# Optimization experiments

Hardware: AMD Instinct MI355X
Metric: run time of the kernel (lower is better)

The kernel has to match this reference:

```python
import jax, jax.numpy as jnp
import numpy as np

VOXEL_SIZE = np.array([0.05, 0.05, 0.1], np.float32)
PC_RANGE = np.array([0.0, -40.0, -3.0, 70.4, 40.0, 1.0], np.float32)
GRID = np.round((PC_RANGE[3:] - PC_RANGE[:3]) / VOXEL_SIZE).astype(np.int64)  # (x,y,z) = (1408,1600,40)
MAX_POINTS = 35
MAX_VOXELS = 60000
N_POINTS = 2_000_000
NDIM = 4


def setup_inputs() -> dict:
    key = jax.random.key(0)
    k1, k2 = jax.random.split(key)
    span = jnp.asarray(PC_RANGE[3:] - PC_RANGE[:3])
    lo = jnp.asarray(PC_RANGE[:3])
    # uniform xyz inside the point-cloud range (slight overshoot ok; out-of-range points get dropped)
    xyz = jax.random.uniform(k1, (N_POINTS, 3), jnp.float32) * span * 1.02 + lo - 0.01 * span
    feat = jax.random.uniform(k2, (N_POINTS, NDIM - 3), jnp.float32)
    return {"points": jnp.concatenate([xyz, feat], axis=1)}


def hard_voxelize(points):
    """Faithful jit-able hard voxelization.

    Returns fixed-size (padded) outputs plus voxel_num, instead of the
    dynamically-sliced outputs of the CUDA kernel (data-dependent shapes are
    not jit-compatible). voxels[:voxel_num], coors[:voxel_num],
    num_points_per_voxel[:voxel_num] match the kernel semantics: voxels are
    numbered in order of first point appearance, points fill a voxel in
    arrival order, overflow points/voxels are dropped.
    """
    n = points.shape[0]
    gx, gy, gz = int(GRID[0]), int(GRID[1]), int(GRID[2])
    c = jnp.floor((points[:, :3] - jnp.asarray(PC_RANGE[:3])) / jnp.asarray(VOXEL_SIZE)).astype(jnp.int32)
    in_range = jnp.all((c >= 0) & (c < jnp.array([gx, gy, gz], jnp.int32)), axis=1)
    big = gx * gy * gz  # sentinel linear id for invalid points
    lin = jnp.where(in_range, (c[:, 2] * gy + c[:, 1]) * gx + c[:, 0], big)

    order = jnp.argsort(lin)  # stable: preserves arrival order within a voxel
    slin = lin[order]
    sc = c[order]
    spts = points[order]

    newg = jnp.concatenate([jnp.ones((1,), bool), slin[1:] != slin[:-1]])
    gid = jnp.cumsum(newg) - 1  # group id per sorted point (sorted-lin order)
    ar = jnp.arange(n, dtype=jnp.int32)

    grp_start = jnp.full((n,), n, jnp.int32).at[gid].min(ar)                      # sorted pos of first pt in group
    first_orig = jnp.full((n,), n, jnp.int32).at[gid].min(order.astype(jnp.int32))  # first-appearance index
    grp_valid = (jnp.zeros((n,), jnp.int32).at[gid].max((slin != big).astype(jnp.int32))) > 0

    # voxel ids assigned in order of first appearance (invalid groups pushed last)
    first_key = jnp.where(grp_valid, first_orig, n)
    perm = jnp.argsort(first_key)
    vid_of_group = jnp.zeros((n,), jnp.int32).at[perm].set(ar)

    pos = ar - grp_start[gid]          # arrival rank of point within its voxel
    vid_pt = vid_of_group[gid]
    keep = (slin != big) & (vid_pt < MAX_VOXELS) & (pos < MAX_POINTS)
    vi = jnp.where(keep, vid_pt, MAX_VOXELS)  # out-of-range -> dropped by scatter
    pi = jnp.where(keep, pos, 0)
    voxels = jnp.zeros((MAX_VOXELS, MAX_POINTS, points.shape[1]), points.dtype).at[vi, pi].set(spts, mode='drop')

    counts = jnp.zeros((n,), jnp.int32).at[gid].add((slin != big).astype(jnp.int32))
    g_ok = grp_valid & (vid_of_group < MAX_VOXELS)
    gv = jnp.where(g_ok, vid_of_group, MAX_VOXELS)
    numpv = jnp.zeros((MAX_VOXELS,), jnp.int32).at[gv].set(jnp.minimum(counts, MAX_POINTS), mode='drop')

    coors_g = sc[jnp.minimum(grp_start, n - 1)][:, ::-1]  # stored as (z, y, x) like the kernel
    coors = jnp.zeros((MAX_VOXELS, 3), jnp.int32).at[gv].set(coors_g, mode='drop')

    voxel_num = jnp.minimum(jnp.sum(grp_valid.astype(jnp.int32)), MAX_VOXELS)
    return voxels, coors, numpv, voxel_num


def reference(points):
    return hard_voxelize(points)
```

## Files before the change

### kernel.cpp

```cpp
#include <hip/hip_runtime.h>

constexpr int GX = 1408, GY = 1600, GZ = 40;
constexpr float LOX = 0.0f, LOY = -40.0f, LOZ = -3.0f;
constexpr float VSX = 0.05f, VSY = 0.05f, VSZ = 0.1f;
constexpr int MAXV = 60000, MAXP = 35;
constexpr int LINBITS = 27;
constexpr unsigned LINMASK = (1u << LINBITS) - 1;
constexpr unsigned EMPTYK = 0xFFFFFFFFu;
constexpr unsigned VINIT  = 0x7FFFFFFFu;

constexpr int NBIN   = 2048;
constexpr int LSLOT  = 2048;
constexpr int BINCAP = 1536;
constexpr int BPT    = 1024;
constexpr int PPB    = 8192;
constexpr int RND    = PPB / BPT;
constexpr int HPT    = BINCAP / 256;

constexpr int NCAND = 131072;
constexpr int NCB   = NCAND / 16384;

constexpr size_t CO_OFF = (size_t)MAXV * MAXP * 4;
constexpr size_t NP_OFF = CO_OFF + (size_t)MAXV * 3;
constexpr size_t VN_OFF = NP_OFF + (size_t)MAXV;

__device__ __forceinline__ unsigned hash22(unsigned lin) {
    return (lin * 2654435761u) >> 10;
}

__global__ __launch_bounds__(1024) void k_bin(const float4* __restrict__ pts, int n,
                                              unsigned long long* __restrict__ binbuf,
                                              int* __restrict__ bincnt) {
    __shared__ int cnt[NBIN], gbase[NBIN];
    int t = threadIdx.x;
    for (int b = t; b < NBIN; b += BPT) cnt[b] = 0;
    __syncthreads();

    unsigned lin[RND];
    unsigned rb[RND];
    int base = blockIdx.x * PPB;
    #pragma unroll
    for (int k = 0; k < RND; ++k) {
        int i = base + k * BPT + t;
        rb[k] = 0xFFFFFFFFu;
        if (i < n) {
            float4 p = pts[i];
            float fx = floorf((p.x - LOX) / VSX);
            float fy = floorf((p.y - LOY) / VSY);
            float fz = floorf((p.z - LOZ) / VSZ);
            if (fx >= 0.f && fy >= 0.f && fz >= 0.f &&
                fx < (float)GX && fy < (float)GY && fz < (float)GZ) {
                unsigned lv = ((unsigned)(int)fz * GY + (unsigned)(int)fy) * GX
                            + (unsigned)(int)fx;
                unsigned b = hash22(lv) >> 11;
                unsigned r = (unsigned)atomicAdd(&cnt[b], 1);
                rb[k] = (b << 16) | r;
                lin[k] = lv;
            }
        }
    }
    __syncthreads();
    for (int b = t; b < NBIN; b += BPT)
        if (cnt[b] > 0) gbase[b] = atomicAdd(&bincnt[b], cnt[b]);
    __syncthreads();
    #pragma unroll
    for (int k = 0; k < RND; ++k) {
        if (rb[k] != 0xFFFFFFFFu) {
            unsigned b = rb[k] >> 16;
            int d = gbase[b] + (int)(rb[k] & 0xFFFFu);
            unsigned i = (unsigned)(base + k * BPT + t);
            if (d < BINCAP)
                binbuf[(size_t)b * BINCAP + d] =
                    ((unsigned long long)i << LINBITS) | lin[k];
        }
    }
}

__device__ __forceinline__ unsigned lds_insert32(unsigned* kt, unsigned* vt,
                                                 unsigned lin, unsigned idx) {
    unsigned h = hash22(lin) & (LSLOT - 1);
    while (true) {
        unsigned k = kt[h];
        if (k == EMPTYK) {
            unsigned old = atomicCAS(&kt[h], EMPTYK, lin);
            if (old == EMPTYK || old == lin) { atomicMin(&vt[h], idx); return h; }
            k = old;
        }
        if (k == lin) { atomicMin(&vt[h], idx); return h; }
        h = (h + 1) & (LSLOT - 1);
    }
}

__global__ __launch_bounds__(256) void k_flags2(const unsigned long long* __restrict__ binbuf,
                                                const int* __restrict__ bincnt,
                                                unsigned char* __restrict__ flagbyte,
                                                int* __restrict__ dcount) {
    __shared__ unsigned kt[LSLOT], vt[LSLOT];
    int t = threadIdx.x, bin = blockIdx.x;
    for (int s = t; s < LSLOT; s += 256) { kt[s] = EMPTYK; vt[s] = VINIT; }
    __syncthreads();
    int cnt = min(bincnt[bin], BINCAP);
    const unsigned long long* buf = binbuf + (size_t)bin * BINCAP;
    for (int j = t; j < cnt; j += 256) {
        unsigned long long e = buf[j];
        lds_insert32(kt, vt, (unsigned)(e & LINMASK), (unsigned)(e >> LINBITS));
    }
    __syncthreads();
    int occ = 0;
    for (int s = t; s < LSLOT; s += 256) {
        if (kt[s] != EMPTYK) {
            ++occ;
            unsigned fi = vt[s];
            if (fi < (unsigned)NCAND) flagbyte[fi] = 1;
        }
    }
    for (int o = 1; o < 64; o <<= 1) occ += __shfl_xor(occ, o);
    __shared__ int ws[4];
    int lane = t & 63, wid = t >> 6;
    if (lane == 0) ws[wid] = occ;
    __syncthreads();
    if (t == 0) atomicAdd(dcount, ws[0] + ws[1] + ws[2] + ws[3]);
}

__device__ __forceinline__ unsigned nib(unsigned v) {
    return (v & 1u) | ((v >> 7) & 2u) | ((v >> 14) & 4u) | ((v >> 21) & 8u);
}

__global__ __launch_bounds__(256) void k_pack(const uint4* __restrict__ fb4,
                                              unsigned* __restrict__ flagw,
                                              int* __restrict__ wsums) {
    int gt = blockIdx.x * 256 + threadIdx.x;
    uint4 q0 = fb4[gt * 4 + 0], q1 = fb4[gt * 4 + 1];
    uint4 q2 = fb4[gt * 4 + 2], q3 = fb4[gt * 4 + 3];
    unsigned w0 = nib(q0.x) | (nib(q0.y) << 4) | (nib(q0.z) << 8)  | (nib(q0.w) << 12)
                | (nib(q1.x) << 16) | (nib(q1.y) << 20) | (nib(q1.z) << 24) | (nib(q1.w) << 28);
    unsigned w1 = nib(q2.x) | (nib(q2.y) << 4) | (nib(q2.z) << 8)  | (nib(q2.w) << 12)
                | (nib(q3.x) << 16) | (nib(q3.y) << 20) | (nib(q3.z) << 24) | (nib(q3.w) << 28);
    flagw[gt * 2]     = w0;
    flagw[gt * 2 + 1] = w1;
    int pc = __popc(w0) + __popc(w1);
    for (int o = 1; o < 64; o <<= 1) pc += __shfl_xor(pc, o);
    __shared__ int ws[4];
    int lane = threadIdx.x & 63, wid = threadIdx.x >> 6;
    if (lane == 0) ws[wid] = pc;
    __syncthreads();
    if (threadIdx.x == 0) wsums[blockIdx.x] = ws[0] + ws[1] + ws[2] + ws[3];
}

__global__ __launch_bounds__(256) void k_wbase(const unsigned* __restrict__ flagw,
                                               const int* __restrict__ wsums,
                                               int* __restrict__ wordbase,
                                               int nb3, const int* __restrict__ dcount,
                                               float* __restrict__ vn_out) {
    __shared__ int sh[256];
    int t = threadIdx.x;
    int v = (t < nb3) ? wsums[t] : 0;
    sh[t] = v;
    __syncthreads();
    for (int o = 1; o < 256; o <<= 1) {
        int u = (t >= o) ? sh[t - o] : 0;
        __syncthreads();
        sh[t] += u;
        __syncthreads();
    }
    int blkbase = (blockIdx.x == 0) ? 0 : sh[blockIdx.x - 1];
    if (blockIdx.x == 0 && t == 0)
        vn_out[0] = (float)min(dcount[0], MAXV);
    __syncthreads();
    int gt = blockIdx.x * 256 + t;
    unsigned w0 = flagw[gt * 2], w1 = flagw[gt * 2 + 1];
    int p0 = __popc(w0);
    int mysum = p0 + __popc(w1);
    sh[t] = mysum;
    __syncthreads();
    for (int o = 1; o < 256; o <<= 1) {
        int u = (t >= o) ? sh[t - o] : 0;
        __syncthreads();
        sh[t] += u;
        __syncthreads();
    }
    int excl = sh[t] - mysum + blkbase;
    wordbase[gt * 2]     = excl;
    wordbase[gt * 2 + 1] = excl + p0;
}

__global__ __launch_bounds__(256) void k_fill2(const unsigned long long* __restrict__ binbuf,
                                               const int* __restrict__ bincnt,
                                               const unsigned* __restrict__ flagw,
                                               const int* __restrict__ wordbase,
                                               int* __restrict__ cursor,
                                               int* __restrict__ lists,
                                               float* __restrict__ coors_out) {
    __shared__ unsigned kt[LSLOT], vt[LSLOT];
    int t = threadIdx.x, bin = blockIdx.x;
    for (int s = t; s < LSLOT; s += 256) { kt[s] = EMPTYK; vt[s] = VINIT; }
    __syncthreads();
    int cnt = min(bincnt[bin], BINCAP);
    const unsigned long long* buf = binbuf + (size_t)bin * BINCAP;
    unsigned hmem[HPT];
    #pragma unroll
    for (int q = 0; q < HPT; ++q) {
        int j = t + q * 256;
        hmem[q] = 0;
        if (j < cnt) {
            unsigned long long e = buf[j];
            hmem[q] = lds_insert32(kt, vt, (unsigned)(e & LINMASK),
                                   (unsigned)(e >> LINBITS));
        }
    }
    __syncthreads();
    for (int s = t; s < LSLOT; s += 256) {
        unsigned k = kt[s];
        if (k == EMPTYK) continue;
        unsigned fi = vt[s];
        unsigned vid = (unsigned)MAXV;
        if (fi < (unsigned)NCAND) {
            unsigned w = flagw[fi >> 5];
            vid = (unsigned)wordbase[fi >> 5]
                + (unsigned)__popc(w & ((1u << (fi & 31)) - 1u));
        }
        vt[s] = vid;
        if (vid < (unsigned)MAXV) {
            int x = (int)(k % (unsigned)GX);
            unsigned tq = k / (unsigned)GX;
            coors_out[(size_t)vid * 3 + 0] = (float)(tq / (unsigned)GY);
            coors_out[(size_t)vid * 3 + 1] = (float)(tq % (unsigned)GY);
            coors_out[(size_t)vid * 3 + 2] = (float)x;
        }
    }
    __syncthreads();
    #pragma unroll
    for (int q = 0; q < HPT; ++q) {
        int j = t + q * 256;
        if (j < cnt) {
            unsigned vid = vt[hmem[q]];
            if (vid < (unsigned)MAXV) {
                unsigned i = (unsigned)(buf[j] >> LINBITS);
                int pos = atomicAdd(&cursor[vid], 1);
                if (pos < MAXP) lists[vid * MAXP + pos] = (int)i;
            }
        }
    }
}

constexpr int VPB = 7;
__global__ __launch_bounds__(256) void k_write(const int* __restrict__ cursor,
                                               const int* __restrict__ lists,
                                               const float4* __restrict__ pts,
                                               float* __restrict__ vox_out,
                                               float* __restrict__ np_out) {
    __shared__ int sidx[VPB * MAXP];
    __shared__ int scnt[VPB];
    int t = threadIdx.x;
    int lv = t / MAXP;
    int r  = t - lv * MAXP;
    int v  = blockIdx.x * VPB + lv;
    bool act = (t < VPB * MAXP) && (v < MAXV);
    if (act && r == 0) scnt[lv] = min(cursor[v], MAXP);
    __syncthreads();
    int k = 0, myidx = 0x7fffffff;
    if (act) {
        k = scnt[lv];
        if (r < k) myidx = lists[v * MAXP + r];
        sidx[lv * MAXP + r] = myidx;
    }
    __syncthreads();
    if (!act) return;
    float4 val = make_float4(0.f, 0.f, 0.f, 0.f);
    int rank = r;
    if (r < k) {
        rank = 0;
        for (int j = 0; j < k; ++j) rank += (sidx[lv * MAXP + j] < myidx);
        val = pts[myidx];
    }
    ((float4*)vox_out)[(size_t)v * MAXP + rank] = val;
    if (r == 0) np_out[v] = (float)k;
}

extern "C" void kernel_launch(void* const* d_in, const int* in_sizes, int n_in,
                              void* d_out, int out_size, void* d_ws, size_t ws_size,
                              hipStream_t stream) {
    const float4* pts = (const float4*)d_in[0];
    int n = in_sizes[0] / 4;
    float* out = (float*)d_out;
    char* ws = (char*)d_ws;
    int nbin_blk = (n + PPB - 1) / PPB;

    size_t off = 0;
    unsigned char* flagbyte = (unsigned char*)(ws + off);
    off += (size_t)NCAND;
    int* cursor = (int*)(ws + off);
    off += (size_t)MAXV * 4;
    int* bincnt = (int*)(ws + off);
    off += (size_t)NBIN * 4;
    int* dcount = (int*)(ws + off);
    off += 256;
    size_t zero_bytes = off;
    off = (off + 255) & ~(size_t)255;
    unsigned long long* binbuf = (unsigned long long*)(ws + off);
    off += (size_t)NBIN * BINCAP * 8;
    unsigned* flagw = (unsigned*)(ws + off);
    off += (size_t)NCB * 512 * 4;
    int* wordbase = (int*)(ws + off);
    off += (size_t)NCB * 512 * 4;
    int* wsums = (int*)(ws + off);
    off += 1024;
    int* lists = (int*)(ws + off);

    hipMemsetAsync(flagbyte, 0, zero_bytes, stream);
    hipMemsetAsync(out + CO_OFF, 0, (size_t)(out_size - (int)CO_OFF) * 4, stream);

    k_bin   <<<nbin_blk, BPT, 0, stream>>>(pts, n, binbuf, bincnt);
    k_flags2<<<NBIN, 256, 0, stream>>>(binbuf, bincnt, flagbyte, dcount);
    k_pack  <<<NCB, 256, 0, stream>>>((const uint4*)flagbyte, flagw, wsums);
    k_wbase <<<NCB, 256, 0, stream>>>(flagw, wsums, wordbase, NCB, dcount, out + VN_OFF);
    k_fill2 <<<NBIN, 256, 0, stream>>>(binbuf, bincnt, flagw, wordbase,
                                       cursor, lists, out + CO_OFF);
    k_write <<<(MAXV + VPB - 1) / VPB, 256, 0, stream>>>(cursor, lists, pts,
                                                         out, out + NP_OFF);
}
```

Before: 176.6 us.

## Persist per-point first-index from hash pass and merge flag pack/scan into one kernel

The first hash-table pass now writes each point's voxel first-appearance index to a global per-bin array, so the fill kernel no longer rebuilds the LDS hash table and just looks up the voxel id per point. The flag packing and the two-level prefix scan are merged into a single one-block kernel, which cuts one launch. In exchange it adds an extra 4-byte global write and read per binned point, and the scan now runs on a single workgroup.

New measurement: 165.4 us. -6.3%, faster.

```diff
diff --git a/kernel.cpp b/kernel.cpp
--- a/kernel.cpp
+++ b/kernel.cpp
@@ -18,7 +18,6 @@
 constexpr int HPT    = BINCAP / 256;
 
 constexpr int NCAND = 131072;
-constexpr int NCB   = NCAND / 16384;
 
 constexpr size_t CO_OFF = (size_t)MAXV * MAXP * 4;
 constexpr size_t NP_OFF = CO_OFF + (size_t)MAXV * 3;
@@ -91,19 +90,29 @@
     }
 }
 
-__global__ __launch_bounds__(256) void k_flags2(const unsigned long long* __restrict__ binbuf,
-                                                const int* __restrict__ bincnt,
-                                                unsigned char* __restrict__ flagbyte,
-                                                int* __restrict__ dcount) {
+__global__ __launch_bounds__(256) void k_tab(const unsigned long long* __restrict__ binbuf,
+                                             const int* __restrict__ bincnt,
+                                             unsigned char* __restrict__ flagbyte,
+                                             unsigned* __restrict__ pfirst,
+                                             int* __restrict__ dcount) {
     __shared__ unsigned kt[LSLOT], vt[LSLOT];
+    __shared__ int ws4[4];
     int t = threadIdx.x, bin = blockIdx.x;
+    int lane = t & 63, wid = t >> 6;
     for (int s = t; s < LSLOT; s += 256) { kt[s] = EMPTYK; vt[s] = VINIT; }
     __syncthreads();
     int cnt = min(bincnt[bin], BINCAP);
     const unsigned long long* buf = binbuf + (size_t)bin * BINCAP;
-    for (int j = t; j < cnt; j += 256) {
-        unsigned long long e = buf[j];
-        lds_insert32(kt, vt, (unsigned)(e & LINMASK), (unsigned)(e >> LINBITS));
+    unsigned mem[HPT];
+    #pragma unroll
+    for (int q = 0; q < HPT; ++q) {
+        int j = t + q * 256;
+        mem[q] = 0;
+        if (j < cnt) {
+            unsigned long long e = buf[j];
+            mem[q] = lds_insert32(kt, vt, (unsigned)(e & LINMASK),
+                                  (unsigned)(e >> LINBITS));
+        }
     }
     __syncthreads();
     int occ = 0;
@@ -115,47 +124,40 @@
         }
     }
     for (int o = 1; o < 64; o <<= 1) occ += __shfl_xor(occ, o);
-    __shared__ int ws[4];
-    int lane = t & 63, wid = t >> 6;
-    if (lane == 0) ws[wid] = occ;
-    __syncthreads();
-    if (t == 0) atomicAdd(dcount, ws[0] + ws[1] + ws[2] + ws[3]);
+    if (lane == 0) ws4[wid] = occ;
+    unsigned* pf = pfirst + (size_t)bin * BINCAP;
+    #pragma unroll
+    for (int q = 0; q < HPT; ++q) {
+        int j = t + q * 256;
+        if (j < cnt) pf[j] = vt[mem[q]];
+    }
+    __syncthreads();
+    if (t == 0) atomicAdd(dcount, ws4[0] + ws4[1] + ws4[2] + ws4[3]);
 }
 
 __device__ __forceinline__ unsigned nib(unsigned v) {
     return (v & 1u) | ((v >> 7) & 2u) | ((v >> 14) & 4u) | ((v >> 21) & 8u);
 }
 
-__global__ __launch_bounds__(256) void k_pack(const uint4* __restrict__ fb4,
-                                              unsigned* __restrict__ flagw,
-                                              int* __restrict__ wsums) {
-    int gt = blockIdx.x * 256 + threadIdx.x;
-    uint4 q0 = fb4[gt * 4 + 0], q1 = fb4[gt * 4 + 1];
-    uint4 q2 = fb4[gt * 4 + 2], q3 = fb4[gt * 4 + 3];
-    unsigned w0 = nib(q0.x) | (nib(q0.y) << 4) | (nib(q0.z) << 8)  | (nib(q0.w) << 12)
-                | (nib(q1.x) << 16) | (nib(q1.y) << 20) | (nib(q1.z) << 24) | (nib(q1.w) << 28);
-    unsigned w1 = nib(q2.x) | (nib(q2.y) << 4) | (nib(q2.z) << 8)  | (nib(q2.w) << 12)
-                | (nib(q3.x) << 16) | (nib(q3.y) << 20) | (nib(q3.z) << 24) | (nib(q3.w) << 28);
-    flagw[gt * 2]     = w0;
-    flagw[gt * 2 + 1] = w1;
-    int pc = __popc(w0) + __popc(w1);
-    for (int o = 1; o < 64; o <<= 1) pc += __shfl_xor(pc, o);
-    __shared__ int ws[4];
-    int lane = threadIdx.x & 63, wid = threadIdx.x >> 6;
-    if (lane == 0) ws[wid] = pc;
-    __syncthreads();
-    if (threadIdx.x == 0) wsums[blockIdx.x] = ws[0] + ws[1] + ws[2] + ws[3];
-}
-
-__global__ __launch_bounds__(256) void k_wbase(const unsigned* __restrict__ flagw,
-                                               const int* __restrict__ wsums,
+__global__ __launch_bounds__(256) void k_scan1(const uint4* __restrict__ fb4,
+                                               unsigned* __restrict__ flagw,
                                                int* __restrict__ wordbase,
-                                               int nb3, const int* __restrict__ dcount,
+                                               const int* __restrict__ dcount,
                                                float* __restrict__ vn_out) {
     __shared__ int sh[256];
     int t = threadIdx.x;
-    int v = (t < nb3) ? wsums[t] : 0;
-    sh[t] = v;
+    unsigned w[16];
+    int mysum = 0;
+    int b4 = t * 32;
+    #pragma unroll
+    for (int k = 0; k < 16; ++k) {
+        uint4 a = fb4[b4 + 2 * k], b = fb4[b4 + 2 * k + 1];
+        unsigned wk = nib(a.x) | (nib(a.y) << 4) | (nib(a.z) << 8)  | (nib(a.w) << 12)
+                    | (nib(b.x) << 16) | (nib(b.y) << 20) | (nib(b.z) << 24) | (nib(b.w) << 28);
+        w[k] = wk;
+        mysum += __popc(wk);
+    }
+    sh[t] = mysum;
     __syncthreads();
     for (int o = 1; o < 256; o <<= 1) {
         int u = (t >= o) ? sh[t - o] : 0;
@@ -163,83 +165,47 @@
         sh[t] += u;
         __syncthreads();
     }
-    int blkbase = (blockIdx.x == 0) ? 0 : sh[blockIdx.x - 1];
-    if (blockIdx.x == 0 && t == 0)
-        vn_out[0] = (float)min(dcount[0], MAXV);
-    __syncthreads();
-    int gt = blockIdx.x * 256 + t;
-    unsigned w0 = flagw[gt * 2], w1 = flagw[gt * 2 + 1];
-    int p0 = __popc(w0);
-    int mysum = p0 + __popc(w1);
-    sh[t] = mysum;
-    __syncthreads();
-    for (int o = 1; o < 256; o <<= 1) {
-        int u = (t >= o) ? sh[t - o] : 0;
-        __syncthreads();
-        sh[t] += u;
-        __syncthreads();
-    }
-    int excl = sh[t] - mysum + blkbase;
-    wordbase[gt * 2]     = excl;
-    wordbase[gt * 2 + 1] = excl + p0;
-}
-
-__global__ __launch_bounds__(256) void k_fill2(const unsigned long long* __restrict__ binbuf,
+    int run = sh[t] - mysum;
+    if (t == 0) vn_out[0] = (float)min(dcount[0], MAXV);
+    #pragma unroll
+    for (int k = 0; k < 16; ++k) {
+        flagw[t * 16 + k] = w[k];
+        wordbase[t * 16 + k] = run;
+        run += __popc(w[k]);
+    }
+}
+
+__global__ __launch_bounds__(256) void k_fill3(const unsigned long long* __restrict__ binbuf,
                                                const int* __restrict__ bincnt,
+                                               const unsigned* __restrict__ pfirst,
                                                const unsigned* __restrict__ flagw,
                                                const int* __restrict__ wordbase,
                                                int* __restrict__ cursor,
                                                int* __restrict__ lists,
                                                float* __restrict__ coors_out) {
-    __shared__ unsigned kt[LSLOT], vt[LSLOT];
     int t = threadIdx.x, bin = blockIdx.x;
-    for (int s = t; s < LSLOT; s += 256) { kt[s] = EMPTYK; vt[s] = VINIT; }
-    __syncthreads();
     int cnt = min(bincnt[bin], BINCAP);
     const unsigned long long* buf = binbuf + (size_t)bin * BINCAP;
-    unsigned hmem[HPT];
-    #pragma unroll
-    for (int q = 0; q < HPT; ++q) {
-        int j = t + q * 256;
-        hmem[q] = 0;
-        if (j < cnt) {
-            unsigned long long e = buf[j];
-            hmem[q] = lds_insert32(kt, vt, (unsigned)(e & LINMASK),
-                                   (unsigned)(e >> LINBITS));
-        }
-    }
-    __syncthreads();
-    for (int s = t; s < LSLOT; s += 256) {
-        unsigned k = kt[s];
-        if (k == EMPTYK) continue;
-        unsigned fi = vt[s];
-        unsigned vid = (unsigned)MAXV;
-        if (fi < (unsigned)NCAND) {
-            unsigned w = flagw[fi >> 5];
-            vid = (unsigned)wordbase[fi >> 5]
-                + (unsigned)__popc(w & ((1u << (fi & 31)) - 1u));
-        }
-        vt[s] = vid;
-        if (vid < (unsigned)MAXV) {
-            int x = (int)(k % (unsigned)GX);
-            unsigned tq = k / (unsigned)GX;
+    const unsigned* pf = pfirst + (size_t)bin * BINCAP;
+    for (int j = t; j < cnt; j += 256) {
+        unsigned long long e = buf[j];
+        unsigned idx = (unsigned)(e >> LINBITS);
+        unsigned fi  = pf[j];
+        if (fi >= (unsigned)NCAND) continue;
+        unsigned wv = flagw[fi >> 5];
+        unsigned vid = (unsigned)wordbase[fi >> 5]
+                     + (unsigned)__popc(wv & ((1u << (fi & 31)) - 1u));
+        if (vid >= (unsigned)MAXV) continue;
+        if (idx == fi) {
+            unsigned lin = (unsigned)(e & LINMASK);
+            int x = (int)(lin % (unsigned)GX);
+            unsigned tq = lin / (unsigned)GX;
             coors_out[(size_t)vid * 3 + 0] = (float)(tq / (unsigned)GY);
             coors_out[(size_t)vid * 3 + 1] = (float)(tq % (unsigned)GY);
             coors_out[(size_t)vid * 3 + 2] = (float)x;
         }
-    }
-    __syncthreads();
-    #pragma unroll
-    for (int q = 0; q < HPT; ++q) {
-        int j = t + q * 256;
-        if (j < cnt) {
-            unsigned vid = vt[hmem[q]];
-            if (vid < (unsigned)MAXV) {
-                unsigned i = (unsigned)(buf[j] >> LINBITS);
-                int pos = atomicAdd(&cursor[vid], 1);
-                if (pos < MAXP) lists[vid * MAXP + pos] = (int)i;
-            }
-        }
+        int pos = atomicAdd(&cursor[vid], 1);
+        if (pos < MAXP) lists[vid * MAXP + pos] = (int)idx;
     }
 }
 
@@ -299,23 +265,23 @@
     off = (off + 255) & ~(size_t)255;
     unsigned long long* binbuf = (unsigned long long*)(ws + off);
     off += (size_t)NBIN * BINCAP * 8;
+    unsigned* pfirst = (unsigned*)(ws + off);
+    off += (size_t)NBIN * BINCAP * 4;
     unsigned* flagw = (unsigned*)(ws + off);
-    off += (size_t)NCB * 512 * 4;
+    off += (size_t)(NCAND / 32) * 4;
     int* wordbase = (int*)(ws + off);
-    off += (size_t)NCB * 512 * 4;
-    int* wsums = (int*)(ws + off);
-    off += 1024;
+    off += (size_t)(NCAND / 32) * 4;
     int* lists = (int*)(ws + off);
 
     hipMemsetAsync(flagbyte, 0, zero_bytes, stream);
     hipMemsetAsync(out + CO_OFF, 0, (size_t)(out_size - (int)CO_OFF) * 4, stream);
 
-    k_bin   <<<nbin_blk, BPT, 0, stream>>>(pts, n, binbuf, bincnt);
-    k_flags2<<<NBIN, 256, 0, stream>>>(binbuf, bincnt, flagbyte, dcount);
-    k_pack  <<<NCB, 256, 0, stream>>>((const uint4*)flagbyte, flagw, wsums);
-    k_wbase <<<NCB, 256, 0, stream>>>(flagw, wsums, wordbase, NCB, dcount, out + VN_OFF);
-    k_fill2 <<<NBIN, 256, 0, stream>>>(binbuf, bincnt, flagw, wordbase,
-                                       cursor, lists, out + CO_OFF);
-    k_write <<<(MAXV + VPB - 1) / VPB, 256, 0, stream>>>(cursor, lists, pts,
-                                                         out, out + NP_OFF);
-}
+    k_bin  <<<nbin_blk, BPT, 0, stream>>>(pts, n, binbuf, bincnt);
+    k_tab  <<<NBIN, 256, 0, stream>>>(binbuf, bincnt, flagbyte, pfirst, dcount);
+    k_scan1<<<1, 256, 0, stream>>>((const uint4*)flagbyte, flagw, wordbase,
+                                   dcount, out + VN_OFF);
+    k_fill3<<<NBIN, 256, 0, stream>>>(binbuf, bincnt, pfirst, flagw, wordbase,
+                                      cursor, lists, out + CO_OFF);
+    k_write<<<(MAXV + VPB - 1) / VPB, 256, 0, stream>>>(cursor, lists, pts,
+                                                        out, out + NP_OFF);
+}
```
